# Kernel optimization log

Measured on AMD Instinct MI355X. Metric: run time of the kernel, lower is better.

## Reference

```python
import jax, jax.numpy as jnp
import numpy as np

N_HEAD = 16
HEAD_DIM = 64  # n_embd // n_head = 1024 // 16


def setup_inputs() -> dict:
    key = jax.random.key(0)
    k1, k2, k3 = jax.random.split(key, 3)
    B, T, C = 4, 2048, 1024
    x = jax.random.normal(k1, (B, T, C), dtype=jnp.float32)
    # torch Linear weight is (out, in); we store transposed (in, out) for x @ W
    w_qkv = jax.random.normal(k2, (C, 3 * C), dtype=jnp.float32) * (1.0 / np.sqrt(C))
    w_out = jax.random.normal(k3, (C, C), dtype=jnp.float32) * (1.0 / np.sqrt(C))
    return {"x": x, "w_qkv": w_qkv, "w_out": w_out}


def reference(x, w_qkv, w_out):
    B, T, C = x.shape
    scale = 1.0 / np.sqrt(HEAD_DIM).astype(np.float32)
    qkv = x @ w_qkv                                   # [B, T, 3C]
    q, k, v = jnp.split(qkv, 3, axis=2)
    def heads(t):  # [B, T, C] -> [B, H, T, Dh]
        return t.reshape(B, T, N_HEAD, HEAD_DIM).transpose(0, 2, 1, 3)
    q, k, v = heads(q), heads(k), heads(v)
    att = jnp.einsum('bhqd,bhkd->bhqk', q, k) * scale  # [B, H, T, T]
    causal = jnp.tril(jnp.ones((T, T), dtype=bool))
    att = jnp.where(causal[None, None], att, jnp.float32(-jnp.inf))
    att = jax.nn.softmax(att, axis=-1)
    y = jnp.einsum('bhqk,bhkd->bhqd', att, v)          # [B, H, T, Dh]
    y = y.transpose(0, 2, 1, 3).reshape(B, T, C)
    return y @ w_out
```

## Files before the change

### kernel.cpp

```cpp
#include <hip/hip_runtime.h>
#include <hip/hip_bf16.h>

#define B_ 4
#define T_ 2048
#define C_ 1024
#define H_ 16
#define D_ 64

typedef __bf16 bf16x8 __attribute__((ext_vector_type(8)));
typedef float f32x4 __attribute__((ext_vector_type(4)));

__device__ __forceinline__ unsigned short f2bs(float f) {
    __hip_bfloat16 h = __float2bfloat16(f);
    return *reinterpret_cast<unsigned short*>(&h);
}

__device__ __forceinline__ int swz(int row, int col) {
    return (row * 64 + col) ^ ((row & 7) << 3);
}

__device__ __forceinline__ void gload16(const void* g, void* l) {
    auto gp = (const __attribute__((address_space(1))) void*)(g);
    auto lp = (__attribute__((address_space(3))) void*)(uintptr_t)(l);
    __builtin_amdgcn_global_load_lds(gp, lp, 16, 0, 0);
}

__global__ __launch_bounds__(256)
void cvt_f32_to_bf16(const float* __restrict__ in, unsigned short* __restrict__ out, int n4) {
    int i = blockIdx.x * 256 + threadIdx.x;
    if (i >= n4) return;
    float4 v = ((const float4*)in)[i];
    union { unsigned short h[4]; uint2 u; } pk;
    pk.h[0] = f2bs(v.x); pk.h[1] = f2bs(v.y);
    pk.h[2] = f2bs(v.z); pk.h[3] = f2bs(v.w);
    ((uint2*)out)[i] = pk.u;
}

__global__ __launch_bounds__(256)
void transpose_weights(const float* __restrict__ in1, unsigned short* __restrict__ out1,
                       const float* __restrict__ in2, unsigned short* __restrict__ out2) {
    __shared__ float tile[64][65];
    const int tx = threadIdx.x & 63;
    const int ty = threadIdx.x >> 6;
    const bool second = blockIdx.x >= 48;
    const float* in = second ? in2 : in1;
    unsigned short* out = second ? out2 : out1;
    const int C = second ? 1024 : 3072;
    const int R = 1024;
    const int c0 = (second ? (blockIdx.x - 48) : blockIdx.x) * 64;
    const int r0 = blockIdx.y * 64;
    #pragma unroll
    for (int i = 0; i < 16; ++i) {
        int r = ty * 16 + i;
        tile[r][tx] = in[(size_t)(r0 + r) * C + c0 + tx];
    }
    __syncthreads();
    #pragma unroll
    for (int i = 0; i < 16; ++i) {
        int r = ty * 16 + i;
        out[(size_t)(c0 + r) * R + r0 + tx] = f2bs(tile[tx][r]);
    }
}

template<int MODE>
__global__ __launch_bounds__(256)
void gemm_bt(const unsigned short* __restrict__ A,
             const unsigned short* __restrict__ Bt,
             float* __restrict__ Out, int N_out,
             unsigned short* __restrict__ Qb,
             unsigned short* __restrict__ Kb,
             unsigned short* __restrict__ Vt,
             int K) {
    __shared__ alignas(16) unsigned short As[2][128 * 64];
    __shared__ alignas(16) unsigned short Bs[2][128 * 64];
    const int tid = threadIdx.x;
    const int l = tid & 63;
    const int c16 = l & 15, lq = l >> 4;
    const int wv = tid >> 6;
    const int wrow = wv >> 1, wcol = wv & 1;
    const int m0 = blockIdx.x * 128, n0 = blockIdx.y * 128;

    f32x4 acc[4][4];
    #pragma unroll
    for (int i = 0; i < 4; ++i)
        #pragma unroll
        for (int j = 0; j < 4; ++j)
            acc[i][j] = f32x4{0.f, 0.f, 0.f, 0.f};

    const int srow = tid >> 3;
    const int scs  = tid & 7;
    const int ldsbase = (tid & ~63) * 8;

    auto stage = [&](int k0, int buf) {
        #pragma unroll
        for (int p = 0; p < 4; ++p) {
            int row = p * 32 + srow;
            int csw = 8 * (scs ^ (row & 7));
            gload16(&A[(size_t)(m0 + row) * K + k0 + csw], &As[buf][p * 2048 + ldsbase]);
            gload16(&Bt[(size_t)(n0 + row) * K + k0 + csw], &Bs[buf][p * 2048 + ldsbase]);
        }
    };

    stage(0, 0);
    const int NK = K >> 6;
    for (int i = 0; i < NK; ++i) {
        __syncthreads();
        if (i + 1 < NK) stage((i + 1) << 6, (i + 1) & 1);
        const unsigned short* Al = As[i & 1];
        const unsigned short* Bl = Bs[i & 1];
        #pragma unroll
        for (int kk = 0; kk < 64; kk += 32) {
            bf16x8 af[4], bfv[4];
            int koff = kk + lq * 8;
            #pragma unroll
            for (int t = 0; t < 4; ++t) {
                af[t]  = *(const bf16x8*)&Al[swz(wrow * 64 + t * 16 + c16, koff)];
                bfv[t] = *(const bf16x8*)&Bl[swz(wcol * 64 + t * 16 + c16, koff)];
            }
            #pragma unroll
            for (int mi = 0; mi < 4; ++mi)
                #pragma unroll
                for (int ni = 0; ni < 4; ++ni)
                    acc[mi][ni] = __builtin_amdgcn_mfma_f32_16x16x32_bf16(
                        af[mi], bfv[ni], acc[mi][ni], 0, 0, 0);
        }
    }

    #pragma unroll
    for (int mi = 0; mi < 4; ++mi) {
        #pragma unroll
        for (int ni = 0; ni < 4; ++ni) {
            #pragma unroll
            for (int r = 0; r < 4; ++r) {
                float v = acc[mi][ni][r];
                int row = m0 + wrow * 64 + mi * 16 + lq * 4 + r;
                int col = n0 + wcol * 64 + ni * 16 + c16;
                if (MODE == 1) {
                    Out[(size_t)row * N_out + col] = v;
                } else {
                    int which = col >> 10;
                    int c = col & 1023;
                    int h = c >> 6, d = c & 63;
                    int b = row >> 11, t = row & 2047;
                    int bh = b * H_ + h;
                    if (which == 0)
                        Qb[((size_t)(bh * T_ + t)) * D_ + d] = f2bs(v * 0.1803368801111204f);
                    else if (which == 1)
                        Kb[((size_t)(bh * T_ + t)) * D_ + d] = f2bs(v);
                    else
                        Vt[((size_t)(bh * D_ + d)) * T_ + t] = f2bs(v);
                }
            }
        }
    }
}

__global__ __launch_bounds__(256, 4)
void attn_fwd(const unsigned short* __restrict__ Qb,
              const unsigned short* __restrict__ Kb,
              const unsigned short* __restrict__ Vt,
              unsigned short* __restrict__ Y) {
    __shared__ alignas(16) unsigned short Ks[2][64 * 64];
    __shared__ alignas(16) unsigned short Vs[2][64 * 64];
    __shared__ alignas(16) unsigned short Pl[4][16 * 64];
    const int tid = threadIdx.x;
    const int wv = tid >> 6;
    const int l = tid & 63;
    const int c16 = l & 15, lq = l >> 4;
    const int bh = blockIdx.x & 63;
    const int qp = blockIdx.x >> 6;
    const unsigned short* Kp = Kb + (size_t)bh * T_ * D_;
    const unsigned short* Vp = Vt + (size_t)bh * D_ * T_;
    const unsigned short* Qbase = Qb + (size_t)bh * T_ * D_;
    const int b = bh >> 4, h = bh & 15;
    const int srow = tid >> 3;
    const int scs  = tid & 7;
    const int scol_sw = 8 * (scs ^ (srow & 7));
    const int wbase = wv * 512;
    unsigned short* Pw = (unsigned short*)Pl[wv];

    #pragma unroll
    for (int half = 0; half < 2; ++half) {
        const int qc = (half == 0) ? qp : 31 - qp;
        const int q0w = qc * 64 + wv * 16;
        const int nt = qc + 1;

        bf16x8 qf[2];
        #pragma unroll
        for (int ks = 0; ks < 2; ++ks)
            qf[ks] = *(const bf16x8*)&Qbase[(size_t)(q0w + c16) * 64 + 32 * ks + 8 * lq];

        f32x4 o[4];
        #pragma unroll
        for (int d0 = 0; d0 < 4; ++d0) o[d0] = f32x4{0.f, 0.f, 0.f, 0.f};
        float lsum = 0.f;

        __syncthreads();
        gload16(&Kp[(size_t)srow * 64 + scol_sw],        &Ks[0][wbase]);
        gload16(&Kp[(size_t)(srow + 32) * 64 + scol_sw], &Ks[0][2048 + wbase]);
        gload16(&Vp[(size_t)srow * T_ + scol_sw],        &Vs[0][wbase]);
        gload16(&Vp[(size_t)(srow + 32) * T_ + scol_sw], &Vs[0][2048 + wbase]);

        for (int it = 0; it < nt; ++it) {
            const int kb = it * 64;
            __syncthreads();
            if (it + 1 < nt) {
                const int kn = kb + 64;
                unsigned short* Kd = Ks[(it + 1) & 1];
                unsigned short* Vd = Vs[(it + 1) & 1];
                gload16(&Kp[(size_t)(kn + srow) * 64 + scol_sw],        &Kd[wbase]);
                gload16(&Kp[(size_t)(kn + srow + 32) * 64 + scol_sw],   &Kd[2048 + wbase]);
                gload16(&Vp[(size_t)srow * T_ + kn + scol_sw],          &Vd[wbase]);
                gload16(&Vp[(size_t)(srow + 32) * T_ + kn + scol_sw],   &Vd[2048 + wbase]);
            }
            const unsigned short* Kl = Ks[it & 1];
            const unsigned short* Vl = Vs[it & 1];

            f32x4 s[4];
            #pragma unroll
            for (int hh = 0; hh < 4; ++hh) s[hh] = f32x4{0.f, 0.f, 0.f, 0.f};
            __builtin_amdgcn_s_setprio(1);
            #pragma unroll
            for (int ks = 0; ks < 2; ++ks) {
                bf16x8 af[4];
                #pragma unroll
                for (int hh = 0; hh < 4; ++hh)
                    af[hh] = *(const bf16x8*)&Kl[swz(16 * hh + c16, 32 * ks + 8 * lq)];
                #pragma unroll
                for (int hh = 0; hh < 4; ++hh)
                    s[hh] = __builtin_amdgcn_mfma_f32_16x16x32_bf16(af[hh], qf[ks], s[hh], 0, 0, 0);
            }
            __builtin_amdgcn_s_setprio(0);
            if (it == nt - 1) {
                const int q = q0w + c16;
                #pragma unroll
                for (int hh = 0; hh < 4; ++hh)
                    #pragma unroll
                    for (int r = 0; r < 4; ++r)
                        if (kb + 16 * hh + 4 * lq + r > q) s[hh][r] = -1e30f;
            }
            float rs = 0.f;
            #pragma unroll
            for (int hh = 0; hh < 4; ++hh)
                #pragma unroll
                for (int r = 0; r < 4; ++r) {
                    float p = exp2f(s[hh][r]);
                    s[hh][r] = p;
                    rs += p;
                }
            lsum += rs;
            #pragma unroll
            for (int hh = 0; hh < 4; ++hh) {
                uint2 pk;
                pk.x = (unsigned)f2bs(s[hh][0]) | ((unsigned)f2bs(s[hh][1]) << 16);
                pk.y = (unsigned)f2bs(s[hh][2]) | ((unsigned)f2bs(s[hh][3]) << 16);
                *(uint2*)&Pw[swz(c16, 16 * hh + 4 * lq)] = pk;
            }
            __builtin_amdgcn_s_setprio(1);
            #pragma unroll
            for (int ks = 0; ks < 2; ++ks) {
                bf16x8 pb = *(const bf16x8*)&Pw[swz(c16, 32 * ks + 8 * lq)];
                #pragma unroll
                for (int d0 = 0; d0 < 4; ++d0) {
                    bf16x8 va = *(const bf16x8*)&Vl[swz(16 * d0 + c16, 32 * ks + 8 * lq)];
                    o[d0] = __builtin_amdgcn_mfma_f32_16x16x32_bf16(va, pb, o[d0], 0, 0, 0);
                }
            }
            __builtin_amdgcn_s_setprio(0);
        }

        float lt = lsum;
        lt += __shfl_xor(lt, 16);
        lt += __shfl_xor(lt, 32);
        float inv = 1.f / lt;
        int t = q0w + c16;
        #pragma unroll
        for (int d0 = 0; d0 < 4; ++d0) {
            uint2 w;
            w.x = (unsigned)f2bs(o[d0][0] * inv) | ((unsigned)f2bs(o[d0][1] * inv) << 16);
            w.y = (unsigned)f2bs(o[d0][2] * inv) | ((unsigned)f2bs(o[d0][3] * inv) << 16);
            *(uint2*)&Y[((size_t)(b * T_ + t)) * C_ + h * D_ + 16 * d0 + 4 * lq] = w;
        }
    }
}

extern "C" void kernel_launch(void* const* d_in, const int* in_sizes, int n_in,
                              void* d_out, int out_size, void* d_ws, size_t ws_size,
                              hipStream_t stream) {
    const float* x     = (const float*)d_in[0];
    const float* w_qkv = (const float*)d_in[1];
    const float* w_out = (const float*)d_in[2];
    float* out = (float*)d_out;
    char* ws = (char*)d_ws;

    unsigned short* xb  = (unsigned short*)(ws);
    unsigned short* wqt = (unsigned short*)(ws + (16u << 20));
    unsigned short* wot = (unsigned short*)(ws + (22u << 20));
    unsigned short* Qb  = (unsigned short*)(ws + (24u << 20));
    unsigned short* Kb  = (unsigned short*)(ws + (40u << 20));
    unsigned short* Vt  = (unsigned short*)(ws + (56u << 20));
    unsigned short* Yb  = (unsigned short*)(ws + (72u << 20));

    cvt_f32_to_bf16<<<8192, 256, 0, stream>>>(x, xb, (B_ * T_ * C_) / 4);
    transpose_weights<<<dim3(64, 16), 256, 0, stream>>>(w_qkv, wqt, w_out, wot);
    gemm_bt<0><<<dim3(64, 24), 256, 0, stream>>>(xb, wqt, nullptr, 3072, Qb, Kb, Vt, 1024);
    attn_fwd<<<1024, 256, 0, stream>>>(Qb, Kb, Vt, Yb);
    gemm_bt<1><<<dim3(64, 8), 256, 0, stream>>>(Yb, wot, out, 1024, nullptr, nullptr, nullptr, 1024);
}
```

Measured before the change: 179.3 us.

## Switch attention to 32x32x16 MFMA with register P via permlane swap

The attention kernel now uses 32x32x16 bf16 MFMA tiles, with each wave handling 32 query rows and each block 128 queries, which halves the grid. The softmax probabilities are packed with v_cvt_pk_bf16_f32 and rearranged in registers via permlane32 swaps instead of a round trip through LDS. Fully masked key tiles are skipped per wave. This aims to raise MFMA efficiency and remove LDS traffic for P, but it lowers occupancy through the 2-wave launch bound and larger tiles, and adds per-wave imbalance on the causal diagonal.

New measurement: 171.2 us. 4.6% less time.

```diff
diff --git a/kernel.cpp b/kernel.cpp
--- a/kernel.cpp
+++ b/kernel.cpp
@@ -9,10 +9,31 @@
 
 typedef __bf16 bf16x8 __attribute__((ext_vector_type(8)));
 typedef float f32x4 __attribute__((ext_vector_type(4)));
+typedef float f32x16 __attribute__((ext_vector_type(16)));
 
 __device__ __forceinline__ unsigned short f2bs(float f) {
     __hip_bfloat16 h = __float2bfloat16(f);
     return *reinterpret_cast<unsigned short*>(&h);
+}
+
+__device__ __forceinline__ unsigned cvtpk(float a, float b) {
+    unsigned r;
+    asm("v_cvt_pk_bf16_f32 %0, %1, %2" : "=v"(r) : "v"(a), "v"(b));
+    return r;
+}
+
+__device__ __forceinline__ void plane32swap(unsigned& a, unsigned& b, int hi) {
+#if __has_builtin(__builtin_amdgcn_permlane32_swap)
+    typedef int i32x2 __attribute__((ext_vector_type(2)));
+    i32x2 r = __builtin_amdgcn_permlane32_swap((int)a, (int)b, false, false);
+    a = (unsigned)r.x; b = (unsigned)r.y;
+#else
+    unsigned v = hi ? a : b;
+    unsigned e = __shfl_xor(v, 32);
+    unsigned na = hi ? e : a;
+    unsigned nb = hi ? b : e;
+    a = na; b = nb;
+#endif
 }
 
 __device__ __forceinline__ int swz(int row, int col) {
@@ -155,18 +176,19 @@
     }
 }
 
-__global__ __launch_bounds__(256, 4)
+__global__ __launch_bounds__(256, 2)
 void attn_fwd(const unsigned short* __restrict__ Qb,
               const unsigned short* __restrict__ Kb,
               const unsigned short* __restrict__ Vt,
               unsigned short* __restrict__ Y) {
     __shared__ alignas(16) unsigned short Ks[2][64 * 64];
     __shared__ alignas(16) unsigned short Vs[2][64 * 64];
-    __shared__ alignas(16) unsigned short Pl[4][16 * 64];
     const int tid = threadIdx.x;
     const int wv = tid >> 6;
     const int l = tid & 63;
-    const int c16 = l & 15, lq = l >> 4;
+    const int r32 = l & 31;
+    const int hi = l >> 5;
+    const int hi8 = hi * 8;
     const int bh = blockIdx.x & 63;
     const int qp = blockIdx.x >> 6;
     const unsigned short* Kp = Kb + (size_t)bh * T_ * D_;
@@ -177,22 +199,22 @@
     const int scs  = tid & 7;
     const int scol_sw = 8 * (scs ^ (srow & 7));
     const int wbase = wv * 512;
-    unsigned short* Pw = (unsigned short*)Pl[wv];
 
     #pragma unroll
     for (int half = 0; half < 2; ++half) {
-        const int qc = (half == 0) ? qp : 31 - qp;
-        const int q0w = qc * 64 + wv * 16;
-        const int nt = qc + 1;
-
-        bf16x8 qf[2];
-        #pragma unroll
-        for (int ks = 0; ks < 2; ++ks)
-            qf[ks] = *(const bf16x8*)&Qbase[(size_t)(q0w + c16) * 64 + 32 * ks + 8 * lq];
-
-        f32x4 o[4];
-        #pragma unroll
-        for (int d0 = 0; d0 < 4; ++d0) o[d0] = f32x4{0.f, 0.f, 0.f, 0.f};
+        const int qc = (half == 0) ? qp : 15 - qp;
+        const int q0w = qc * 128 + wv * 32;
+        const int nt = 2 * qc + 2;
+        const int qg = q0w + r32;
+
+        bf16x8 qf[4];
+        #pragma unroll
+        for (int ds = 0; ds < 4; ++ds)
+            qf[ds] = *(const bf16x8*)&Qbase[(size_t)qg * 64 + ds * 16 + hi8];
+
+        f32x16 o[2];
+        #pragma unroll
+        for (int e = 0; e < 16; ++e) { o[0][e] = 0.f; o[1][e] = 0.f; }
         float lsum = 0.f;
 
         __syncthreads();
@@ -213,74 +235,79 @@
                 gload16(&Vp[(size_t)srow * T_ + kn + scol_sw],          &Vd[wbase]);
                 gload16(&Vp[(size_t)(srow + 32) * T_ + kn + scol_sw],   &Vd[2048 + wbase]);
             }
+            if (kb > q0w + 31) continue;
             const unsigned short* Kl = Ks[it & 1];
             const unsigned short* Vl = Vs[it & 1];
 
-            f32x4 s[4];
-            #pragma unroll
-            for (int hh = 0; hh < 4; ++hh) s[hh] = f32x4{0.f, 0.f, 0.f, 0.f};
+            f32x16 s[2];
+            #pragma unroll
+            for (int e = 0; e < 16; ++e) { s[0][e] = 0.f; s[1][e] = 0.f; }
             __builtin_amdgcn_s_setprio(1);
             #pragma unroll
-            for (int ks = 0; ks < 2; ++ks) {
-                bf16x8 af[4];
-                #pragma unroll
-                for (int hh = 0; hh < 4; ++hh)
-                    af[hh] = *(const bf16x8*)&Kl[swz(16 * hh + c16, 32 * ks + 8 * lq)];
-                #pragma unroll
-                for (int hh = 0; hh < 4; ++hh)
-                    s[hh] = __builtin_amdgcn_mfma_f32_16x16x32_bf16(af[hh], qf[ks], s[hh], 0, 0, 0);
-            }
+            for (int kt = 0; kt < 2; ++kt)
+                #pragma unroll
+                for (int ds = 0; ds < 4; ++ds) {
+                    bf16x8 af = *(const bf16x8*)&Kl[swz(32 * kt + r32, ds * 16 + hi8)];
+                    s[kt] = __builtin_amdgcn_mfma_f32_32x32x16_bf16(af, qf[ds], s[kt], 0, 0, 0);
+                }
             __builtin_amdgcn_s_setprio(0);
-            if (it == nt - 1) {
-                const int q = q0w + c16;
-                #pragma unroll
-                for (int hh = 0; hh < 4; ++hh)
+            if (kb + 63 > q0w) {
+                #pragma unroll
+                for (int kt = 0; kt < 2; ++kt)
                     #pragma unroll
-                    for (int r = 0; r < 4; ++r)
-                        if (kb + 16 * hh + 4 * lq + r > q) s[hh][r] = -1e30f;
+                    for (int m = 0; m < 4; ++m)
+                        #pragma unroll
+                        for (int r = 0; r < 4; ++r)
+                            if (kb + 32 * kt + 8 * m + r + 4 * hi > qg)
+                                s[kt][4 * m + r] = -1e30f;
             }
             float rs = 0.f;
             #pragma unroll
-            for (int hh = 0; hh < 4; ++hh)
-                #pragma unroll
-                for (int r = 0; r < 4; ++r) {
-                    float p = exp2f(s[hh][r]);
-                    s[hh][r] = p;
+            for (int kt = 0; kt < 2; ++kt)
+                #pragma unroll
+                for (int e = 0; e < 16; ++e) {
+                    float p = exp2f(s[kt][e]);
+                    s[kt][e] = p;
                     rs += p;
                 }
             lsum += rs;
-            #pragma unroll
-            for (int hh = 0; hh < 4; ++hh) {
-                uint2 pk;
-                pk.x = (unsigned)f2bs(s[hh][0]) | ((unsigned)f2bs(s[hh][1]) << 16);
-                pk.y = (unsigned)f2bs(s[hh][2]) | ((unsigned)f2bs(s[hh][3]) << 16);
-                *(uint2*)&Pw[swz(c16, 16 * hh + 4 * lq)] = pk;
+            bf16x8 pb[4];
+            #pragma unroll
+            for (int ks = 0; ks < 4; ++ks) {
+                const int kt = ks >> 1;
+                const int m0 = (ks & 1) * 2;
+                unsigned a0 = cvtpk(s[kt][4 * m0 + 0], s[kt][4 * m0 + 1]);
+                unsigned a1 = cvtpk(s[kt][4 * m0 + 2], s[kt][4 * m0 + 3]);
+                unsigned b0 = cvtpk(s[kt][4 * m0 + 4], s[kt][4 * m0 + 5]);
+                unsigned b1 = cvtpk(s[kt][4 * m0 + 6], s[kt][4 * m0 + 7]);
+                plane32swap(a0, b0, hi);
+                plane32swap(a1, b1, hi);
+                uint4 u = {a0, a1, b0, b1};
+                pb[ks] = *reinterpret_cast<bf16x8*>(&u);
             }
             __builtin_amdgcn_s_setprio(1);
             #pragma unroll
-            for (int ks = 0; ks < 2; ++ks) {
-                bf16x8 pb = *(const bf16x8*)&Pw[swz(c16, 32 * ks + 8 * lq)];
-                #pragma unroll
-                for (int d0 = 0; d0 < 4; ++d0) {
-                    bf16x8 va = *(const bf16x8*)&Vl[swz(16 * d0 + c16, 32 * ks + 8 * lq)];
-                    o[d0] = __builtin_amdgcn_mfma_f32_16x16x32_bf16(va, pb, o[d0], 0, 0, 0);
+            for (int dt = 0; dt < 2; ++dt)
+                #pragma unroll
+                for (int ks = 0; ks < 4; ++ks) {
+                    bf16x8 va = *(const bf16x8*)&Vl[swz(32 * dt + r32, ks * 16 + hi8)];
+                    o[dt] = __builtin_amdgcn_mfma_f32_32x32x16_bf16(va, pb[ks], o[dt], 0, 0, 0);
                 }
-            }
             __builtin_amdgcn_s_setprio(0);
         }
 
-        float lt = lsum;
-        lt += __shfl_xor(lt, 16);
-        lt += __shfl_xor(lt, 32);
+        float lt = lsum + __shfl_xor(lsum, 32);
         float inv = 1.f / lt;
-        int t = q0w + c16;
-        #pragma unroll
-        for (int d0 = 0; d0 < 4; ++d0) {
-            uint2 w;
-            w.x = (unsigned)f2bs(o[d0][0] * inv) | ((unsigned)f2bs(o[d0][1] * inv) << 16);
-            w.y = (unsigned)f2bs(o[d0][2] * inv) | ((unsigned)f2bs(o[d0][3] * inv) << 16);
-            *(uint2*)&Y[((size_t)(b * T_ + t)) * C_ + h * D_ + 16 * d0 + 4 * lq] = w;
-        }
+        #pragma unroll
+        for (int dt = 0; dt < 2; ++dt)
+            #pragma unroll
+            for (int m = 0; m < 4; ++m) {
+                uint2 w;
+                w.x = cvtpk(o[dt][4 * m + 0] * inv, o[dt][4 * m + 1] * inv);
+                w.y = cvtpk(o[dt][4 * m + 2] * inv, o[dt][4 * m + 3] * inv);
+                int d = 32 * dt + 8 * m + 4 * hi;
+                *(uint2*)&Y[((size_t)(b * T_ + qg)) * C_ + h * D_ + d] = w;
+            }
     }
 }
 
@@ -304,6 +331,6 @@
     cvt_f32_to_bf16<<<8192, 256, 0, stream>>>(x, xb, (B_ * T_ * C_) / 4);
     transpose_weights<<<dim3(64, 16), 256, 0, stream>>>(w_qkv, wqt, w_out, wot);
     gemm_bt<0><<<dim3(64, 24), 256, 0, stream>>>(xb, wqt, nullptr, 3072, Qb, Kb, Vt, 1024);
-    attn_fwd<<<1024, 256, 0, stream>>>(Qb, Kb, Vt, Yb);
+    attn_fwd<<<512, 256, 0, stream>>>(Qb, Kb, Vt, Yb);
     gemm_bt<1><<<dim3(64, 8), 256, 0, stream>>>(Yb, wot, out, 1024, nullptr, nullptr, nullptr, 1024);
 }
```
